# Kernel tuning notes

Measured on AMD Instinct MI355X. Metric: run time of the kernel, lower is better.

The kernel has to match this reference:

```python
import jax, jax.numpy as jnp
import numpy as np

NIN = 1024
NOUT = 1024
NHEADS = 16
DHEAD = NOUT // NHEADS


def setup_inputs() -> dict:
    key = jax.random.key(0)
    k1, k2, k3, k4 = jax.random.split(key, 4)
    y = jax.random.normal(k1, (2, 2048, NIN), dtype=jnp.float32)
    Wqkv = jax.random.normal(k2, (NIN, 3 * NOUT), dtype=jnp.float32) * (1.0 / np.sqrt(NIN))
    Wff = jax.random.normal(k3, (NOUT, NOUT), dtype=jnp.float32) * (1.0 / np.sqrt(NOUT))
    bff = jax.random.normal(k4, (NOUT,), dtype=jnp.float32) * 0.01
    return {"y": y, "Wqkv": Wqkv, "Wff": Wff, "bff": bff}


def reference(y, Wqkv, Wff, bff):
    b, n, _ = y.shape
    qkv = y @ Wqkv  # [b, n, 3*nout]
    qkv = qkv.reshape(b, n, 3, NHEADS, DHEAD).transpose(2, 0, 3, 1, 4)
    q, k, v = qkv[0], qkv[1], qkv[2]  # each [b, h, n, d]
    att = jnp.einsum('bhqd,bhkd->bhqk', q, k)
    causal = jnp.triu(jnp.ones((n, n), dtype=bool), k=1)
    att = jnp.where(causal, -jnp.inf, att)
    att = jax.nn.softmax(att / jnp.sqrt(jnp.float32(DHEAD)), axis=-1)
    ctx = jnp.einsum('bhqk,bhkd->bhqd', att, v)
    ctx = ctx.transpose(0, 2, 1, 3).reshape(b, n, NOUT)
    return ctx @ Wff + bff
```

## Files before the change

### kernel.cpp

```cpp
#include <hip/hip_runtime.h>
#include <stdint.h>

#define NHEADS 16
#define DHEAD 64
#define SEQ 2048
#define BATCH 2
#define NINF 1024
#define NOUTF 1024
#define N3 3072
#define MTOT 4096

typedef unsigned short US;
typedef __attribute__((ext_vector_type(8))) short short8;
typedef __attribute__((ext_vector_type(4))) short short4v;
typedef __attribute__((ext_vector_type(4))) float f32x4;

__device__ inline US f2bf(float f) {
  union { float f; unsigned u; } v; v.f = f;
  unsigned r = v.u + 0x7fffu + ((v.u >> 16) & 1u);
  return (US)(r >> 16);
}

__device__ inline f32x4 mfma16(short8 a, short8 b, f32x4 c) {
  return __builtin_amdgcn_mfma_f32_16x16x32_bf16(a, b, c, 0, 0, 0);
}

__device__ inline f32x4 mfma16k16(short4v a, short4v b, f32x4 c) {
  return __builtin_amdgcn_mfma_f32_16x16x16bf16_1k(a, b, c, 0, 0, 0);
}

__device__ inline void async16(const US* g, US* l) {
  __builtin_amdgcn_global_load_lds(
      (const __attribute__((address_space(1))) unsigned int*)g,
      (__attribute__((address_space(3))) unsigned int*)l, 16, 0, 0);
}

__global__ void k_convert(const float* __restrict__ src, US* __restrict__ dst, int n4) {
  int i = blockIdx.x * blockDim.x + threadIdx.x;
  if (i >= n4) return;
  float4 v = ((const float4*)src)[i];
  ushort4 o;
  o.x = f2bf(v.x); o.y = f2bf(v.y); o.z = f2bf(v.z); o.w = f2bf(v.w);
  ((ushort4*)dst)[i] = o;
}

__global__ void k_wtrans(const float* __restrict__ Wqkv, const float* __restrict__ Wff,
                         US* __restrict__ dq, US* __restrict__ df) {
  __shared__ float tile[32][33];
  int bxi = blockIdx.x;
  const float* src; US* dst; int C;
  if (bxi < 96) { src = Wqkv; dst = dq; C = N3; }
  else          { src = Wff;  dst = df; C = NOUTF; bxi -= 96; }
  int bx = bxi * 32, by = blockIdx.y * 32;
  int tx = threadIdx.x, ty = threadIdx.y;
  for (int i = 0; i < 32; i += 8)
    tile[ty + i][tx] = src[(size_t)(by + ty + i) * C + bx + tx];
  __syncthreads();
  for (int i = 0; i < 32; i += 8)
    dst[(size_t)(bx + ty + i) * 1024 + by + tx] = f2bf(tile[tx][ty + i]);
}

__global__ void k_vtrans(const US* __restrict__ src, US* __restrict__ dst) {
  __shared__ US tile[32][33];
  int bh = blockIdx.z;
  int bx = blockIdx.x * 32;
  int by = blockIdx.y * 32;
  int tx = threadIdx.x, ty = threadIdx.y;
  const US* s0 = src + (size_t)bh * SEQ * DHEAD;
  US* d0 = dst + (size_t)bh * DHEAD * SEQ;
  for (int i = 0; i < 32; i += 8)
    tile[ty + i][tx] = s0[(size_t)(by + ty + i) * DHEAD + bx + tx];
  __syncthreads();
  for (int i = 0; i < 32; i += 8)
    d0[(size_t)(bx + ty + i) * SEQ + by + tx] = tile[tx][ty + i];
}

__global__ __launch_bounds__(256) void k_gemm_qkv(
    const US* __restrict__ A,
    const US* __restrict__ Bt,
    US* __restrict__ qbuf, US* __restrict__ kbuf, US* __restrict__ vbuf) {
  __shared__ US As[128 * 32];
  __shared__ US Bs[128 * 32];
  int tid = threadIdx.x;
  int wave = tid >> 6, lane = tid & 63, lm = lane & 15, lk = lane >> 4;
  int wm = wave >> 1, wn = wave & 1;
  int mbase = blockIdx.y * 128, nbase = blockIdx.x * 128;

  f32x4 acc[4][4];
#pragma unroll
  for (int i = 0; i < 4; ++i)
#pragma unroll
    for (int j = 0; j < 4; ++j) acc[i][j] = (f32x4){0.f, 0.f, 0.f, 0.f};

  const US* ga = A + (size_t)(mbase + (tid >> 2)) * NINF + (tid & 3) * 8;
  const US* gb = Bt + (size_t)(nbase + (tid >> 2)) * NINF + (tid & 3) * 8;
  US* la = As + tid * 8;
  US* lb = Bs + tid * 8;

  for (int kt = 0; kt < NINF / 32; ++kt) {
    int ko = kt * 32;
    async16(ga + ko, la);
    async16(ga + ko + (size_t)64 * NINF, la + 64 * 32);
    async16(gb + ko, lb);
    async16(gb + ko + (size_t)64 * NINF, lb + 64 * 32);
    __syncthreads();
    short8 a[4], b[4];
#pragma unroll
    for (int i = 0; i < 4; ++i)
      a[i] = *(const short8*)(As + (wm * 64 + i * 16 + lm) * 32 + lk * 8);
#pragma unroll
    for (int j = 0; j < 4; ++j)
      b[j] = *(const short8*)(Bs + (wn * 64 + j * 16 + lm) * 32 + lk * 8);
#pragma unroll
    for (int i = 0; i < 4; ++i)
#pragma unroll
      for (int j = 0; j < 4; ++j) acc[i][j] = mfma16(a[i], b[j], acc[i][j]);
    __syncthreads();
  }

  int which = nbase >> 10;
  US* dsts = (which == 0) ? qbuf : (which == 1) ? kbuf : vbuf;
  float sc = (which == 0) ? 0.18033688011112042f : 1.f;
#pragma unroll
  for (int j = 0; j < 4; ++j) {
    int col = nbase + wn * 64 + j * 16 + lm;
    int hh = (col & 1023) >> 6;
    int d = col & 63;
#pragma unroll
    for (int i = 0; i < 4; ++i) {
#pragma unroll
      for (int r = 0; r < 4; ++r) {
        int row = mbase + wm * 64 + i * 16 + lk * 4 + r;
        int bb = row >> 11;
        int s = row & (SEQ - 1);
        int bh = bb * NHEADS + hh;
        dsts[((size_t)bh * SEQ + s) * DHEAD + d] = f2bf(acc[i][j][r] * sc);
      }
    }
  }
}

__global__ __launch_bounds__(256) void k_attn(
    const US* __restrict__ qbuf, const US* __restrict__ kbuf,
    const US* __restrict__ vtbuf, US* __restrict__ ctx) {
  __shared__ US Ks[64 * 64];
  __shared__ US Vs[64 * 64];
  int tid = threadIdx.x;
  int w = tid >> 6, lane = tid & 63;
  int lm = lane & 15, lk = lane >> 4;
  int bl = blockIdx.x;
  int xcd = bl & 7, g = bl >> 3;
  int bh = (g & 3) * 8 + xcd;
  int s = 31 - (g >> 2);
  int qb = s * 64 + w * 16;
  int nt = s + 1;

  const US* kbase = kbuf + (size_t)bh * SEQ * DHEAD;
  const US* vtb = vtbuf + (size_t)bh * DHEAD * SEQ;
  const US* qr = qbuf + ((size_t)bh * SEQ + qb + lm) * DHEAD + lk * 8;
  short8 qf0 = *(const short8*)(qr);
  short8 qf1 = *(const short8*)(qr + 32);

  int swz = ((lane & 7) ^ (lane >> 3)) * 8;
  const US* gsrc[4];
  US* ldst[4];
  int step[4];
#pragma unroll
  for (int j = 0; j < 4; ++j) {
    int u = w + 4 * j;
    if (u < 8) {
      gsrc[j] = kbase + (size_t)(u * 8 + (lane >> 3)) * DHEAD + swz;
      ldst[j] = Ks + u * 512 + lane * 8;
      step[j] = 64 * DHEAD;
    } else {
      int i = u - 8;
      gsrc[j] = vtb + (size_t)(i * 8 + (lane >> 3)) * SEQ + swz;
      ldst[j] = Vs + i * 512 + lane * 8;
      step[j] = 64;
    }
  }

  int xorv = lm & 7;
  int ck0 = ((lk) ^ xorv) * 16;
  int ck1 = ((4 + lk) ^ xorv) * 16;
  int cv[4];
#pragma unroll
  for (int kg = 0; kg < 4; ++kg)
    cv[kg] = (((kg * 2 + (lk >> 1)) ^ xorv) * 16) + (lk & 1) * 8;

  f32x4 o[4];
#pragma unroll
  for (int dg = 0; dg < 4; ++dg) o[dg] = (f32x4){0.f, 0.f, 0.f, 0.f};
  f32x4 lacc = (f32x4){0.f, 0.f, 0.f, 0.f};
  const short4v kones = {(short)0x3F80, (short)0x3F80, (short)0x3F80, (short)0x3F80};

  const char* Kc = (const char*)Ks;
  const char* Vc = (const char*)Vs;

  auto body = [&](int kg, bool dm) {
    const char* kr = Kc + (kg * 16 + lm) * 128;
    short8 ka0 = *(const short8*)(kr + ck0);
    short8 ka1 = *(const short8*)(kr + ck1);
    f32x4 st = (f32x4){0.f, 0.f, 0.f, 0.f};
    st = mfma16(ka0, qf0, st);
    st = mfma16(ka1, qf1, st);
    uint32_t ue[4];
#pragma unroll
    for (int r = 0; r < 4; ++r) {
      float v = st[r];
      if (dm && (lk * 4 + r > lm)) v = -INFINITY;
      union { float f; uint32_t u; } cv2;
      cv2.f = exp2f(v);
      ue[r] = cv2.u + 0x8000u;
    }
    union { short4v s4; uint32_t u[2]; } pk;
    pk.u[0] = __builtin_amdgcn_perm(ue[1], ue[0], 0x07060302u);
    pk.u[1] = __builtin_amdgcn_perm(ue[3], ue[2], 0x07060302u);
    lacc = mfma16k16(kones, pk.s4, lacc);
    const char* vr = Vc + lm * 128 + cv[kg];
#pragma unroll
    for (int dg = 0; dg < 4; ++dg) {
      short4v va = *(const short4v*)(vr + dg * 2048);
      o[dg] = mfma16k16(va, pk.s4, o[dg]);
    }
  };

  for (int t = 0; t < nt - 1; ++t) {
    __syncthreads();
#pragma unroll
    for (int j = 0; j < 4; ++j) async16(gsrc[j], ldst[j]);
#pragma unroll
    for (int j = 0; j < 4; ++j) gsrc[j] += step[j];
    __syncthreads();
#pragma unroll
    for (int kg = 0; kg < 4; ++kg) body(kg, false);
  }
  __syncthreads();
#pragma unroll
  for (int j = 0; j < 4; ++j) async16(gsrc[j], ldst[j]);
  __syncthreads();
  for (int kg = 0; kg < w; ++kg) body(kg, false);
  body(w, true);

  float inv = 1.f / lacc[0];

  US* crow = ctx + ((size_t)(bh >> 4) * SEQ + qb + lm) * NOUTF + (bh & 15) * DHEAD;
#pragma unroll
  for (int dg = 0; dg < 4; ++dg) {
    union { short4v s4; uint32_t u[2]; } pk;
    pk.u[0] = (uint32_t)f2bf(o[dg][0] * inv) | ((uint32_t)f2bf(o[dg][1] * inv) << 16);
    pk.u[1] = (uint32_t)f2bf(o[dg][2] * inv) | ((uint32_t)f2bf(o[dg][3] * inv) << 16);
    *(short4v*)(crow + dg * 16 + lk * 4) = pk.s4;
  }
}

__global__ __launch_bounds__(256) void k_gemm_out(
    const US* __restrict__ A, const US* __restrict__ Bt,
    const float* __restrict__ bias, float* __restrict__ out) {
  __shared__ US As[128 * 32];
  __shared__ US Bs[64 * 32];
  int tid = threadIdx.x;
  int wave = tid >> 6, lane = tid & 63, lm = lane & 15, lk = lane >> 4;
  int mbase = blockIdx.y * 128, nbase = blockIdx.x * 64;

  f32x4 acc[2][4];
#pragma unroll
  for (int i = 0; i < 2; ++i)
#pragma unroll
    for (int j = 0; j < 4; ++j) acc[i][j] = (f32x4){0.f, 0.f, 0.f, 0.f};

  const US* ga = A + (size_t)(mbase + (tid >> 2)) * NOUTF + (tid & 3) * 8;
  const US* gb = Bt + (size_t)(nbase + (tid >> 2)) * NOUTF + (tid & 3) * 8;
  US* la = As + tid * 8;
  US* lb = Bs + tid * 8;

  for (int kt = 0; kt < NOUTF / 32; ++kt) {
    int ko = kt * 32;
    async16(ga + ko, la);
    async16(ga + ko + (size_t)64 * NOUTF, la + 64 * 32);
    async16(gb + ko, lb);
    __syncthreads();
    short8 a[2], b[4];
#pragma unroll
    for (int i = 0; i < 2; ++i)
      a[i] = *(const short8*)(As + (wave * 32 + i * 16 + lm) * 32 + lk * 8);
#pragma unroll
    for (int j = 0; j < 4; ++j)
      b[j] = *(const short8*)(Bs + (j * 16 + lm) * 32 + lk * 8);
#pragma unroll
    for (int i = 0; i < 2; ++i)
#pragma unroll
      for (int j = 0; j < 4; ++j) acc[i][j] = mfma16(a[i], b[j], acc[i][j]);
    __syncthreads();
  }

#pragma unroll
  for (int j = 0; j < 4; ++j) {
    int col = nbase + j * 16 + lm;
    float bv = bias[col];
#pragma unroll
    for (int i = 0; i < 2; ++i)
#pragma unroll
      for (int r = 0; r < 4; ++r) {
        int row = mbase + wave * 32 + i * 16 + lk * 4 + r;
        out[(size_t)row * NOUTF + col] = acc[i][j][r] + bv;
      }
  }
}

extern "C" void kernel_launch(void* const* d_in, const int* in_sizes, int n_in,
                              void* d_out, int out_size, void* d_ws, size_t ws_size,
                              hipStream_t stream) {
  const float* y    = (const float*)d_in[0];
  const float* Wqkv = (const float*)d_in[1];
  const float* Wff  = (const float*)d_in[2];
  const float* bff  = (const float*)d_in[3];
  float* out = (float*)d_out;

  char* ws = (char*)d_ws;
  US* ybf   = (US*)(ws);
  US* ctx   = (US*)(ws);
  US* wqkvt = (US*)(ws + (8u << 20));
  US* wfft  = (US*)(ws + (14u << 20));
  US* qbuf  = (US*)(ws + (16u << 20));
  US* kbuf  = (US*)(ws + (24u << 20));
  US* vbuf  = (US*)(ws + (32u << 20));
  US* vtbuf = (US*)(ws + (40u << 20));

  k_convert<<<MTOT * NINF / 4 / 256, 256, 0, stream>>>(y, ybf, MTOT * NINF / 4);
  k_wtrans<<<dim3(128, 32), dim3(32, 8), 0, stream>>>(Wqkv, Wff, wqkvt, wfft);
  k_gemm_qkv<<<dim3(N3 / 128, MTOT / 128), 256, 0, stream>>>(ybf, wqkvt, qbuf, kbuf, vbuf);
  k_vtrans<<<dim3(DHEAD / 32, SEQ / 32, BATCH * NHEADS), dim3(32, 8), 0, stream>>>(vbuf, vtbuf);
  k_attn<<<dim3(1024), 256, 0, stream>>>(qbuf, kbuf, vtbuf, ctx);
  k_gemm_out<<<dim3(NOUTF / 64, MTOT / 128), 256, 0, stream>>>(ctx, wfft, bff, out);
}
```

Baseline: 189.3 us.

## Pair causal query tiles per block and double-buffer K/V loads in attention

Each attention block now handles two query tiles, a short one (pr) and a long one (31-pr), so every block does balanced causal work, and the grid drops from 1024 to 512 blocks. Each loaded K/V tile is reused for both query tiles. K/V tiles are double-buffered in LDS with async loads issued two tiles ahead, using explicit vmcnt waits and raw barriers in place of the load-then-sync pattern. This doubles LDS use and the accumulator registers, which may lower occupancy, and the fewer blocks may underfill the 256 CUs.

```diff
diff --git a/kernel.cpp b/kernel.cpp
--- a/kernel.cpp
+++ b/kernel.cpp
@@ -143,23 +143,27 @@
 __global__ __launch_bounds__(256) void k_attn(
     const US* __restrict__ qbuf, const US* __restrict__ kbuf,
     const US* __restrict__ vtbuf, US* __restrict__ ctx) {
-  __shared__ US Ks[64 * 64];
-  __shared__ US Vs[64 * 64];
+  __shared__ US Ks[2][64 * 64];
+  __shared__ US Vs[2][64 * 64];
   int tid = threadIdx.x;
   int w = tid >> 6, lane = tid & 63;
   int lm = lane & 15, lk = lane >> 4;
   int bl = blockIdx.x;
   int xcd = bl & 7, g = bl >> 3;
   int bh = (g & 3) * 8 + xcd;
-  int s = 31 - (g >> 2);
-  int qb = s * 64 + w * 16;
-  int nt = s + 1;
+  int pr = g >> 2;
+  int sA = pr;
+  int sB = 31 - pr;
+  int nt = sB + 1;
 
   const US* kbase = kbuf + (size_t)bh * SEQ * DHEAD;
   const US* vtb = vtbuf + (size_t)bh * DHEAD * SEQ;
-  const US* qr = qbuf + ((size_t)bh * SEQ + qb + lm) * DHEAD + lk * 8;
-  short8 qf0 = *(const short8*)(qr);
-  short8 qf1 = *(const short8*)(qr + 32);
+  const US* qrA = qbuf + ((size_t)bh * SEQ + sA * 64 + w * 16 + lm) * DHEAD + lk * 8;
+  const US* qrB = qbuf + ((size_t)bh * SEQ + sB * 64 + w * 16 + lm) * DHEAD + lk * 8;
+  short8 qA0 = *(const short8*)(qrA);
+  short8 qA1 = *(const short8*)(qrA + 32);
+  short8 qB0 = *(const short8*)(qrB);
+  short8 qB1 = *(const short8*)(qrB + 32);
 
   int swz = ((lane & 7) ^ (lane >> 3)) * 8;
   const US* gsrc[4];
@@ -170,12 +174,12 @@
     int u = w + 4 * j;
     if (u < 8) {
       gsrc[j] = kbase + (size_t)(u * 8 + (lane >> 3)) * DHEAD + swz;
-      ldst[j] = Ks + u * 512 + lane * 8;
+      ldst[j] = &Ks[0][0] + u * 512 + lane * 8;
       step[j] = 64 * DHEAD;
     } else {
       int i = u - 8;
       gsrc[j] = vtb + (size_t)(i * 8 + (lane >> 3)) * SEQ + swz;
-      ldst[j] = Vs + i * 512 + lane * 8;
+      ldst[j] = &Vs[0][0] + i * 512 + lane * 8;
       step[j] = 64;
     }
   }
@@ -188,22 +192,24 @@
   for (int kg = 0; kg < 4; ++kg)
     cv[kg] = (((kg * 2 + (lk >> 1)) ^ xorv) * 16) + (lk & 1) * 8;
 
-  f32x4 o[4];
-#pragma unroll
-  for (int dg = 0; dg < 4; ++dg) o[dg] = (f32x4){0.f, 0.f, 0.f, 0.f};
-  f32x4 lacc = (f32x4){0.f, 0.f, 0.f, 0.f};
+  f32x4 oA[4], oB[4];
+#pragma unroll
+  for (int dg = 0; dg < 4; ++dg) {
+    oA[dg] = (f32x4){0.f, 0.f, 0.f, 0.f};
+    oB[dg] = (f32x4){0.f, 0.f, 0.f, 0.f};
+  }
+  f32x4 lA = (f32x4){0.f, 0.f, 0.f, 0.f};
+  f32x4 lB = (f32x4){0.f, 0.f, 0.f, 0.f};
   const short4v kones = {(short)0x3F80, (short)0x3F80, (short)0x3F80, (short)0x3F80};
 
-  const char* Kc = (const char*)Ks;
-  const char* Vc = (const char*)Vs;
-
-  auto body = [&](int kg, bool dm) {
+  auto body = [&](const char* Kc, const char* Vc, int kg, bool dm,
+                  short8 q0, short8 q1, f32x4* o, f32x4& ls) {
     const char* kr = Kc + (kg * 16 + lm) * 128;
     short8 ka0 = *(const short8*)(kr + ck0);
     short8 ka1 = *(const short8*)(kr + ck1);
     f32x4 st = (f32x4){0.f, 0.f, 0.f, 0.f};
-    st = mfma16(ka0, qf0, st);
-    st = mfma16(ka1, qf1, st);
+    st = mfma16(ka0, q0, st);
+    st = mfma16(ka1, q1, st);
     uint32_t ue[4];
 #pragma unroll
     for (int r = 0; r < 4; ++r) {
@@ -216,7 +222,7 @@
     union { short4v s4; uint32_t u[2]; } pk;
     pk.u[0] = __builtin_amdgcn_perm(ue[1], ue[0], 0x07060302u);
     pk.u[1] = __builtin_amdgcn_perm(ue[3], ue[2], 0x07060302u);
-    lacc = mfma16k16(kones, pk.s4, lacc);
+    ls = mfma16k16(kones, pk.s4, ls);
     const char* vr = Vc + lm * 128 + cv[kg];
 #pragma unroll
     for (int dg = 0; dg < 4; ++dg) {
@@ -225,32 +231,62 @@
     }
   };
 
-  for (int t = 0; t < nt - 1; ++t) {
-    __syncthreads();
-#pragma unroll
-    for (int j = 0; j < 4; ++j) async16(gsrc[j], ldst[j]);
-#pragma unroll
-    for (int j = 0; j < 4; ++j) gsrc[j] += step[j];
-    __syncthreads();
-#pragma unroll
-    for (int kg = 0; kg < 4; ++kg) body(kg, false);
-  }
-  __syncthreads();
-#pragma unroll
-  for (int j = 0; j < 4; ++j) async16(gsrc[j], ldst[j]);
-  __syncthreads();
-  for (int kg = 0; kg < w; ++kg) body(kg, false);
-  body(w, true);
-
-  float inv = 1.f / lacc[0];
-
-  US* crow = ctx + ((size_t)(bh >> 4) * SEQ + qb + lm) * NOUTF + (bh & 15) * DHEAD;
+  auto doTile = [&](int t) {
+    const char* Kc = (const char*)Ks + (t & 1) * 8192;
+    const char* Vc = (const char*)Vs + (t & 1) * 8192;
+    if (t < sB) {
+#pragma unroll
+      for (int kg = 0; kg < 4; ++kg) body(Kc, Vc, kg, false, qB0, qB1, oB, lB);
+    } else {
+      for (int kg = 0; kg < w; ++kg) body(Kc, Vc, kg, false, qB0, qB1, oB, lB);
+      body(Kc, Vc, w, true, qB0, qB1, oB, lB);
+    }
+    if (t < sA) {
+#pragma unroll
+      for (int kg = 0; kg < 4; ++kg) body(Kc, Vc, kg, false, qA0, qA1, oA, lA);
+    } else if (t == sA) {
+      for (int kg = 0; kg < w; ++kg) body(Kc, Vc, kg, false, qA0, qA1, oA, lA);
+      body(Kc, Vc, w, true, qA0, qA1, oA, lA);
+    }
+  };
+
+#pragma unroll
+  for (int j = 0; j < 4; ++j) { async16(gsrc[j], ldst[j]); gsrc[j] += step[j]; }
+#pragma unroll
+  for (int j = 0; j < 4; ++j) { async16(gsrc[j], ldst[j] + 4096); gsrc[j] += step[j]; }
+
+  for (int t = 0; t < nt; ++t) {
+    if (t + 1 < nt) asm volatile("s_waitcnt vmcnt(4)" ::: "memory");
+    else            asm volatile("s_waitcnt vmcnt(0)" ::: "memory");
+    __builtin_amdgcn_s_barrier();
+    asm volatile("" ::: "memory");
+    doTile(t);
+    asm volatile("" ::: "memory");
+    __builtin_amdgcn_s_barrier();
+    asm volatile("" ::: "memory");
+    if (t + 2 < nt) {
+#pragma unroll
+      for (int j = 0; j < 4; ++j) {
+        async16(gsrc[j], ldst[j] + (t & 1) * 4096);
+        gsrc[j] += step[j];
+      }
+    }
+  }
+
+  float invA = 1.f / lA[0];
+  float invB = 1.f / lB[0];
+
+  US* crowA = ctx + ((size_t)(bh >> 4) * SEQ + sA * 64 + w * 16 + lm) * NOUTF + (bh & 15) * DHEAD;
+  US* crowB = ctx + ((size_t)(bh >> 4) * SEQ + sB * 64 + w * 16 + lm) * NOUTF + (bh & 15) * DHEAD;
 #pragma unroll
   for (int dg = 0; dg < 4; ++dg) {
     union { short4v s4; uint32_t u[2]; } pk;
-    pk.u[0] = (uint32_t)f2bf(o[dg][0] * inv) | ((uint32_t)f2bf(o[dg][1] * inv) << 16);
-    pk.u[1] = (uint32_t)f2bf(o[dg][2] * inv) | ((uint32_t)f2bf(o[dg][3] * inv) << 16);
-    *(short4v*)(crow + dg * 16 + lk * 4) = pk.s4;
+    pk.u[0] = (uint32_t)f2bf(oA[dg][0] * invA) | ((uint32_t)f2bf(oA[dg][1] * invA) << 16);
+    pk.u[1] = (uint32_t)f2bf(oA[dg][2] * invA) | ((uint32_t)f2bf(oA[dg][3] * invA) << 16);
+    *(short4v*)(crowA + dg * 16 + lk * 4) = pk.s4;
+    pk.u[0] = (uint32_t)f2bf(oB[dg][0] * invB) | ((uint32_t)f2bf(oB[dg][1] * invB) << 16);
+    pk.u[1] = (uint32_t)f2bf(oB[dg][2] * invB) | ((uint32_t)f2bf(oB[dg][3] * invB) << 16);
+    *(short4v*)(crowB + dg * 16 + lk * 4) = pk.s4;
   }
 }
 
@@ -331,6 +367,6 @@
   k_wtrans<<<dim3(128, 32), dim3(32, 8), 0, stream>>>(Wqkv, Wff, wqkvt, wfft);
   k_gemm_qkv<<<dim3(N3 / 128, MTOT / 128), 256, 0, stream>>>(ybf, wqkvt, qbuf, kbuf, vbuf);
   k_vtrans<<<dim3(DHEAD / 32, SEQ / 32, BATCH * NHEADS), dim3(32, 8), 0, stream>>>(vbuf, vtbuf);
-  k_attn<<<dim3(1024), 256, 0, stream>>>(qbuf, kbuf, vtbuf, ctx);
+  k_attn<<<dim3(512), 256, 0, stream>>>(qbuf, kbuf, vtbuf, ctx);
   k_gemm_out<<<dim3(NOUTF / 64, MTOT / 128), 256, 0, stream>>>(ctx, wfft, bff, out);
 }
```

After: 190.4 us. Within noise of the previous version (+0.6%).

## Double-buffer K/V tiles in attention and reorder causal block scheduling

Applied to the files above, without the earlier changes.

The attention kernel now keeps two LDS buffers for K and V and issues the async load for tile t+2 while computing on tile t. It waits with explicit vmcnt counters in place of a full sync before each tile, hiding global-load latency behind the MFMA work. The mapping from block to query block is also changed from a plain descending order to an interleaved long/short order, to balance the causal triangle's uneven work across waves of blocks. LDS use doubles, which may lower occupancy, and the hand-written waitcnt logic relies on the exact count of outstanding loads.

```diff
diff --git a/kernel.cpp b/kernel.cpp
--- a/kernel.cpp
+++ b/kernel.cpp
@@ -143,15 +143,17 @@
 __global__ __launch_bounds__(256) void k_attn(
     const US* __restrict__ qbuf, const US* __restrict__ kbuf,
     const US* __restrict__ vtbuf, US* __restrict__ ctx) {
-  __shared__ US Ks[64 * 64];
-  __shared__ US Vs[64 * 64];
+  __shared__ US Ks[2][64 * 64];
+  __shared__ US Vs[2][64 * 64];
   int tid = threadIdx.x;
   int w = tid >> 6, lane = tid & 63;
   int lm = lane & 15, lk = lane >> 4;
   int bl = blockIdx.x;
   int xcd = bl & 7, g = bl >> 3;
   int bh = (g & 3) * 8 + xcd;
-  int s = 31 - (g >> 2);
+  int q4 = g >> 2;
+  int rr = q4 >> 3, qq = q4 & 7;
+  int s = (rr == 0) ? 31 - qq : (rr == 1) ? qq : (rr == 2) ? 23 - qq : 8 + qq;
   int qb = s * 64 + w * 16;
   int nt = s + 1;
 
@@ -170,12 +172,12 @@
     int u = w + 4 * j;
     if (u < 8) {
       gsrc[j] = kbase + (size_t)(u * 8 + (lane >> 3)) * DHEAD + swz;
-      ldst[j] = Ks + u * 512 + lane * 8;
+      ldst[j] = &Ks[0][0] + u * 512 + lane * 8;
       step[j] = 64 * DHEAD;
     } else {
       int i = u - 8;
       gsrc[j] = vtb + (size_t)(i * 8 + (lane >> 3)) * SEQ + swz;
-      ldst[j] = Vs + i * 512 + lane * 8;
+      ldst[j] = &Vs[0][0] + i * 512 + lane * 8;
       step[j] = 64;
     }
   }
@@ -194,10 +196,7 @@
   f32x4 lacc = (f32x4){0.f, 0.f, 0.f, 0.f};
   const short4v kones = {(short)0x3F80, (short)0x3F80, (short)0x3F80, (short)0x3F80};
 
-  const char* Kc = (const char*)Ks;
-  const char* Vc = (const char*)Vs;
-
-  auto body = [&](int kg, bool dm) {
+  auto body = [&](const char* Kc, const char* Vc, int kg, bool dm) {
     const char* kr = Kc + (kg * 16 + lm) * 128;
     short8 ka0 = *(const short8*)(kr + ck0);
     short8 ka1 = *(const short8*)(kr + ck1);
@@ -225,22 +224,38 @@
     }
   };
 
-  for (int t = 0; t < nt - 1; ++t) {
-    __syncthreads();
-#pragma unroll
-    for (int j = 0; j < 4; ++j) async16(gsrc[j], ldst[j]);
-#pragma unroll
-    for (int j = 0; j < 4; ++j) gsrc[j] += step[j];
-    __syncthreads();
-#pragma unroll
-    for (int kg = 0; kg < 4; ++kg) body(kg, false);
-  }
-  __syncthreads();
-#pragma unroll
-  for (int j = 0; j < 4; ++j) async16(gsrc[j], ldst[j]);
-  __syncthreads();
-  for (int kg = 0; kg < w; ++kg) body(kg, false);
-  body(w, true);
+#pragma unroll
+  for (int j = 0; j < 4; ++j) { async16(gsrc[j], ldst[j]); gsrc[j] += step[j]; }
+  if (nt > 1) {
+#pragma unroll
+    for (int j = 0; j < 4; ++j) { async16(gsrc[j], ldst[j] + 4096); gsrc[j] += step[j]; }
+  }
+
+  for (int t = 0; t < nt; ++t) {
+    if (t + 1 < nt) asm volatile("s_waitcnt vmcnt(4)" ::: "memory");
+    else            asm volatile("s_waitcnt vmcnt(0)" ::: "memory");
+    __builtin_amdgcn_s_barrier();
+    asm volatile("" ::: "memory");
+    const char* Kc = (const char*)Ks + (t & 1) * 8192;
+    const char* Vc = (const char*)Vs + (t & 1) * 8192;
+    if (t < s) {
+#pragma unroll
+      for (int kg = 0; kg < 4; ++kg) body(Kc, Vc, kg, false);
+    } else {
+      for (int kg = 0; kg < w; ++kg) body(Kc, Vc, kg, false);
+      body(Kc, Vc, w, true);
+    }
+    asm volatile("" ::: "memory");
+    __builtin_amdgcn_s_barrier();
+    asm volatile("" ::: "memory");
+    if (t + 2 < nt) {
+#pragma unroll
+      for (int j = 0; j < 4; ++j) {
+        async16(gsrc[j], ldst[j] + (t & 1) * 4096);
+        gsrc[j] += step[j];
+      }
+    }
+  }
 
   float inv = 1.f / lacc[0];
 
```

After: 184.1 us. 1.03x faster.
